# Kernel optimization log

Measured on AMD Instinct MI355X. Metric: run time of the kernel, lower is better.

## Reference

```python
import jax, jax.numpy as jnp
import numpy as np
from jax import lax

N = 51200            # total nodes
E = 409600           # edges
FEAT = 768           # BERT emb size
HID = 256            # GGNN out_channels
L = 6                # GGNN layers
NPG = 200            # nodes per graph (conv1d_1 in_channels)
C1_OUT, K1, P1 = 50, 3, 1
C2_OUT, K2 = 20, 1
MP1_K, MP1_S = 3, 2
MP2_K, MP2_S = 2, 2

def _pooled_len(n):
    n = (n - MP1_K) // MP1_S + 1
    n = (n - MP2_K) // MP2_S + 1
    return n

def setup_inputs():
    key = jax.random.key(0)
    ks = jax.random.split(key, 12)
    s = lambda i, shape: jax.random.normal(ks[i], shape, jnp.float32) * 0.02
    fc1_in = C2_OUT * _pooled_len(HID + FEAT)  # 20*255 = 5100
    fc2_in = C2_OUT * _pooled_len(HID)         # 20*63  = 1260
    return dict(
        x=jax.random.normal(ks[0], (N, FEAT), jnp.float32),
        edge_index=jax.random.randint(ks[1], (2, E), 0, N, dtype=jnp.int32),
        W_in=s(2, (HID, FEAT)), b_in=jnp.zeros((HID,), jnp.float32),
        W_ggnn=s(3, (L, HID, HID)),
        W_ih=s(4, (3 * HID, HID)), W_hh=s(5, (3 * HID, HID)),
        b_ih=jnp.zeros((3 * HID,), jnp.float32), b_hh=jnp.zeros((3 * HID,), jnp.float32),
        Wc1=s(6, (C1_OUT, NPG, K1)), bc1=jnp.zeros((C1_OUT,), jnp.float32),
        Wc2=s(7, (C2_OUT, C1_OUT, K2)), bc2=jnp.zeros((C2_OUT,), jnp.float32),
        Wf1=s(8, (1, fc1_in)), bf1=jnp.zeros((1,), jnp.float32),
        Wf2=s(9, (1, fc2_in)), bf2=jnp.zeros((1,), jnp.float32),
    )

def _conv1d(x, w, b, pad):
    y = lax.conv_general_dilated(x, w, (1,), [(pad, pad)], dimension_numbers=('NCH', 'OIH', 'NCH'))
    return y + b[None, :, None]

def _maxpool1d(x, k, s):
    return lax.reduce_window(x, -jnp.inf, lax.max, (1, 1, k), (1, 1, s), 'VALID')

def _ggnn(h0, src, dst, W_ggnn, W_ih, W_hh, b_ih, b_hh):
    h = h0
    for i in range(L):  # fixed small layer loop
        m = h @ W_ggnn[i]                                   # [N, HID]
        agg = jax.ops.segment_sum(m[src], dst, num_segments=N)  # scatter-add aggr
        gi = agg @ W_ih.T + b_ih                            # GRUCell input gates
        gh = h @ W_hh.T + b_hh                              # GRUCell hidden gates
        i_r, i_z, i_n = jnp.split(gi, 3, axis=1)
        h_r, h_z, h_n = jnp.split(gh, 3, axis=1)
        r = jax.nn.sigmoid(i_r + h_r)
        z = jax.nn.sigmoid(i_z + h_z)
        n = jnp.tanh(i_n + r * h_n)
        h = (1.0 - z) * n + z * h
    return h

def _conv_head(h, x, Wc1, bc1, Wc2, bc2, Wf1, bf1, Wf2, bf2):
    concat = jnp.concatenate([h, x], axis=1).reshape(-1, NPG, HID + FEAT)  # [G, NPG, 1024]
    Z = _maxpool1d(jax.nn.relu(_conv1d(concat, Wc1, bc1, P1)), MP1_K, MP1_S)
    Z = _maxpool1d(_conv1d(Z, Wc2, bc2, 0), MP2_K, MP2_S)
    Y = h.reshape(-1, NPG, HID)
    Y = _maxpool1d(jax.nn.relu(_conv1d(Y, Wc1, bc1, P1)), MP1_K, MP1_S)
    Y = _maxpool1d(_conv1d(Y, Wc2, bc2, 0), MP2_K, MP2_S)
    z = Z.reshape(Z.shape[0], -1) @ Wf1.T + bf1
    y = Y.reshape(Y.shape[0], -1) @ Wf2.T + bf2
    # dropout p=0.2 is identity in eval mode
    return jax.nn.sigmoid((z * y).ravel())  # [G]

def reference(x, edge_index, W_in, b_in, W_ggnn, W_ih, W_hh, b_ih, b_hh, Wc1, bc1, Wc2, bc2, Wf1, bf1, Wf2, bf2):
    h0 = x @ W_in.T + b_in
    h = _ggnn(h0, edge_index[0], edge_index[1], W_ggnn, W_ih, W_hh, b_ih, b_hh)
    p = _conv_head(h, x, Wc1, bc1, Wc2, bc2, Wf1, bf1, Wf2, bf2)
    eps = 1e-6
    p = jnp.clip(p, eps, 1.0 - eps)
    z1 = jnp.log(p / (1.0 - p))
    return jnp.stack([jnp.zeros_like(z1), z1], axis=1)  # [G, 2]
```

## Files before the change

kernel.cpp:

```cpp
#include <hip/hip_runtime.h>
#include <math.h>

#define N_NODES 51200
#define N_EDGES 409600
#define FEAT    768
#define HID     256
#define NPG     200
#define G_GRAPHS 256

typedef _Float16 f16x8 __attribute__((ext_vector_type(8)));
typedef _Float16 f16x4 __attribute__((ext_vector_type(4)));
typedef _Float16 f16x2 __attribute__((ext_vector_type(2)));
typedef float    f32x4 __attribute__((ext_vector_type(4)));

__global__ __launch_bounds__(256) void k_deg(const int* __restrict__ ei, int* __restrict__ deg) {
    int e = blockIdx.x * 256 + threadIdx.x;
    if (e < N_EDGES) atomicAdd(&deg[ei[N_EDGES + e]], 1);
}

__global__ __launch_bounds__(1024) void k_scan(const int* __restrict__ deg, int* __restrict__ rowp) {
    __shared__ int sums[1024];
    int tid = threadIdx.x;
    int base = tid * 50;
    int s = 0;
    for (int j = 0; j < 50; ++j) s += deg[base + j];
    sums[tid] = s;
    __syncthreads();
    for (int off = 1; off < 1024; off <<= 1) {
        int v = 0;
        if (tid >= off) v = sums[tid - off];
        __syncthreads();
        sums[tid] += v;
        __syncthreads();
    }
    int run = sums[tid] - s;
    for (int j = 0; j < 50; ++j) { rowp[base + j] = run; run += deg[base + j]; }
    if (tid == 1023) rowp[N_NODES] = run;
}

__global__ __launch_bounds__(256) void k_fill(const int* __restrict__ ei, const int* __restrict__ rowp,
                                              int* __restrict__ fill, int* __restrict__ col) {
    int e = blockIdx.x * 256 + threadIdx.x;
    if (e < N_EDGES) {
        int d = ei[N_EDGES + e];
        int pos = atomicAdd(&fill[d], 1);
        col[rowp[d] + pos] = ei[e];
    }
}

__global__ __launch_bounds__(256) void k_cvt(const float* __restrict__ in, _Float16* __restrict__ out, int n4) {
    int i = blockIdx.x * 256 + threadIdx.x;
    if (i < n4) {
        float4 v = *(const float4*)&in[i * 4];
        f16x4 h;
        h[0] = (_Float16)v.x; h[1] = (_Float16)v.y; h[2] = (_Float16)v.z; h[3] = (_Float16)v.w;
        *(f16x4*)&out[i * 4] = h;
    }
}

__global__ __launch_bounds__(256) void k_bias(const float* __restrict__ bih, const float* __restrict__ bhh,
                                              float* __restrict__ brz) {
    int i = blockIdx.x * 256 + threadIdx.x;
    if (i < 512) brz[i] = bih[i] + bhh[i];
}

__global__ __launch_bounds__(256) void k_bnn(const float* __restrict__ bih, const float* __restrict__ bhh,
                                             float* __restrict__ bnn) {
    int i = blockIdx.x * 256 + threadIdx.x;
    if (i < 512) bnn[i] = (i < 256) ? bih[512 + i] : bhh[512 + (i - 256)];
}

__global__ __launch_bounds__(256) void k_wpack(const float* __restrict__ Wc1, _Float16* __restrict__ Wp) {
    int id = blockIdx.x * 256 + threadIdx.x;
    int ch = id / 12288, r = id - ch * 12288;
    int o = r / 192, k = r - o * 192;
    int dk = k >> 6, cc = k & 63;
    int c = ch * 64 + cc;
    float v = 0.f;
    if (o < 50 && c < NPG) v = Wc1[(o * NPG + c) * 3 + dk];
    Wp[id] = (_Float16)v;
}

__global__ __launch_bounds__(256) void k_wcopyrz(const _Float16* __restrict__ Whh, _Float16* __restrict__ Wrz2) {
    int id = blockIdx.x * 256 + threadIdx.x;
    int l = id >> 17, r = id & 131071;
    int j = r >> 8, c = r & 255;
    Wrz2[(size_t)l * 262144 + j * 512 + 256 + c] = Whh[j * 256 + c];
}

__global__ __launch_bounds__(256) void k_wcopynn(const _Float16* __restrict__ Whh, _Float16* __restrict__ Wnn) {
    int id = blockIdx.x * 256 + threadIdx.x;
    int l = id >> 16, r = id & 65535;
    Wnn[(size_t)l * 131072 + 65536 + r] = Whh[512 * 256 + r];
}

template<int AF16, int OUT, int COLB, int SWZ>
__global__ __launch_bounds__(256) void k_gemm2(const void* __restrict__ Av, int lda,
                                               const _Float16* __restrict__ B,
                                               const float* __restrict__ bias,
                                               void* __restrict__ Cv, int ldc,
                                               _Float16* __restrict__ C2, int ldc2,
                                               int K, int wgPerL, int aLStride, int bLStride,
                                               int cLStride, int biasStride) {
    __shared__ _Float16 As[128 * 64];
    __shared__ _Float16 Bs[128 * 64];
    int wg = blockIdx.x;
    int l = wg / wgPerL; wg -= l * wgPerL;
    if (AF16) Av = (const void*)((const _Float16*)Av + (size_t)l * aLStride);
    else      Av = (const void*)((const float*)Av + (size_t)l * aLStride);
    B += (size_t)l * bLStride;
    if (bias) bias += (size_t)l * biasStride;
    if (OUT == 1) Cv = (void*)((_Float16*)Cv + (size_t)l * cLStride);
    else          Cv = (void*)((float*)Cv + (size_t)l * cLStride);
    int rowBase, colBase;
    if (SWZ) {
        int xcd = wg & 7, t = wg >> 3;
        int cb = t % COLB, gidx = t / COLB;
        rowBase = (gidx * 8 + xcd) * 128;
        colBase = cb * 128;
    } else {
        rowBase = (wg / COLB) * 128;
        colBase = (wg % COLB) * 128;
    }
    int tid = threadIdx.x;
    int lane = tid & 63;
    int wid = tid >> 6;
    int wr = wid >> 1, wc = wid & 1;
    f32x4 acc[4][4] = {};
    for (int k0 = 0; k0 < K; k0 += 64) {
        __syncthreads();
        #pragma unroll
        for (int p = 0; p < 4; ++p) {
            int c = p * 256 + tid;
            int row = c >> 3, slot = c & 7;
            int dst = row * 64 + ((slot ^ (row & 7)) * 8);
            if (AF16) {
                const _Float16* srcA = (const _Float16*)Av + (size_t)(rowBase + row) * lda + k0 + slot * 8;
                *(f16x8*)&As[dst] = *(const f16x8*)srcA;
            } else {
                const float* srcA = (const float*)Av + (size_t)(rowBase + row) * lda + k0 + slot * 8;
                float4 f0 = *(const float4*)srcA;
                float4 f1 = *(const float4*)(srcA + 4);
                f16x8 hv;
                hv[0] = (_Float16)f0.x; hv[1] = (_Float16)f0.y; hv[2] = (_Float16)f0.z; hv[3] = (_Float16)f0.w;
                hv[4] = (_Float16)f1.x; hv[5] = (_Float16)f1.y; hv[6] = (_Float16)f1.z; hv[7] = (_Float16)f1.w;
                *(f16x8*)&As[dst] = hv;
            }
            const _Float16* srcB = B + (size_t)(colBase + row) * K + k0 + slot * 8;
            *(f16x8*)&Bs[dst] = *(const f16x8*)srcB;
        }
        __syncthreads();
        #pragma unroll
        for (int ks = 0; ks < 2; ++ks) {
            f16x8 af[4], bf[4];
            #pragma unroll
            for (int mi = 0; mi < 4; ++mi) {
                int row = wr * 64 + mi * 16 + (lane & 15);
                int slot = (lane >> 4) + ks * 4;
                af[mi] = *(const f16x8*)&As[row * 64 + ((slot ^ (row & 7)) * 8)];
            }
            #pragma unroll
            for (int nj = 0; nj < 4; ++nj) {
                int row = wc * 64 + nj * 16 + (lane & 15);
                int slot = (lane >> 4) + ks * 4;
                bf[nj] = *(const f16x8*)&Bs[row * 64 + ((slot ^ (row & 7)) * 8)];
            }
            #pragma unroll
            for (int mi = 0; mi < 4; ++mi)
                #pragma unroll
                for (int nj = 0; nj < 4; ++nj)
                    acc[mi][nj] = __builtin_amdgcn_mfma_f32_16x16x32_f16(af[mi], bf[nj], acc[mi][nj], 0, 0, 0);
        }
    }
    #pragma unroll
    for (int mi = 0; mi < 4; ++mi) {
        #pragma unroll
        for (int nj = 0; nj < 4; ++nj) {
            int col = colBase + wc * 64 + nj * 16 + (lane & 15);
            float bv = bias ? bias[col] : 0.f;
            #pragma unroll
            for (int r = 0; r < 4; ++r) {
                int row = rowBase + wr * 64 + mi * 16 + (lane >> 4) * 4 + r;
                float val = acc[mi][nj][r] + bv;
                if (OUT == 0) {
                    ((float*)Cv)[(size_t)row * ldc + col] = val;
                } else if (OUT == 1) {
                    ((_Float16*)Cv)[(size_t)row * ldc + col] = (_Float16)val;
                } else {
                    ((float*)Cv)[(size_t)row * ldc + col] = val;
                    C2[(size_t)row * ldc2 + col] = (_Float16)val;
                }
            }
        }
    }
}

__global__ __launch_bounds__(256) void k_agg4(const int* __restrict__ rowp, const int* __restrict__ col,
                                              _Float16* __restrict__ AG) {
    int v = blockIdx.x * 4 + (threadIdx.x >> 6);
    int lane = threadIdx.x & 63;
    int beg = rowp[v], end = rowp[v + 1];
    const _Float16* hf = AG + 256 + lane * 4;
    float a0 = 0.f, a1 = 0.f, a2 = 0.f, a3 = 0.f;
    int i = beg;
    for (; i + 1 < end; i += 2) {
        f16x4 u = *(const f16x4*)&hf[(size_t)col[i] * 512];
        f16x4 w = *(const f16x4*)&hf[(size_t)col[i + 1] * 512];
        a0 += (float)u[0] + (float)w[0];
        a1 += (float)u[1] + (float)w[1];
        a2 += (float)u[2] + (float)w[2];
        a3 += (float)u[3] + (float)w[3];
    }
    if (i < end) {
        f16x4 u = *(const f16x4*)&hf[(size_t)col[i] * 512];
        a0 += (float)u[0]; a1 += (float)u[1]; a2 += (float)u[2]; a3 += (float)u[3];
    }
    f16x4 o;
    o[0] = (_Float16)a0; o[1] = (_Float16)a1; o[2] = (_Float16)a2; o[3] = (_Float16)a3;
    *(f16x4*)&AG[(size_t)v * 512 + lane * 4] = o;
}

__global__ __launch_bounds__(256) void k_gru4(const _Float16* __restrict__ gates, _Float16* __restrict__ AG) {
    int idx = blockIdx.x * 256 + threadIdx.x;
    int n = idx >> 5;
    int c8 = (idx & 31) << 3;
    size_t b = (size_t)n * 1024;
    f16x8 rp = *(const f16x8*)&gates[b + c8];
    f16x8 zp = *(const f16x8*)&gates[b + 256 + c8];
    f16x8 ip = *(const f16x8*)&gates[b + 512 + c8];
    f16x8 hp = *(const f16x8*)&gates[b + 768 + c8];
    f16x8 hv = *(const f16x8*)&AG[(size_t)n * 512 + 256 + c8];
    f16x8 ov;
    #pragma unroll
    for (int q = 0; q < 8; ++q) {
        float r = 1.f / (1.f + expf(-(float)rp[q]));
        float z = 1.f / (1.f + expf(-(float)zp[q]));
        float ng = tanhf((float)ip[q] + r * (float)hp[q]);
        float o = (1.f - z) * ng + z * (float)hv[q];
        ov[q] = (_Float16)o;
    }
    *(f16x8*)&AG[(size_t)n * 512 + 256 + c8] = ov;
}

__global__ __launch_bounds__(256, 2) void k_conv1m(const _Float16* __restrict__ hf, const _Float16* __restrict__ xf,
                                                   const _Float16* __restrict__ Wp, const float* __restrict__ bc1,
                                                   float* __restrict__ out, int H, int TBLK) {
    __shared__ _Float16 XT[272 * 64];
    __shared__ _Float16 WL[64 * 192];
    int g = blockIdx.x / TBLK;
    int tb = blockIdx.x - g * TBLK;
    int t0 = tb * 256;
    int tid = threadIdx.x;
    int lane = tid & 63;
    int wn = (tid >> 6) * 64;
    f32x4 acc[4][4] = {};
    for (int ch = 0; ch < 4; ++ch) {
        __syncthreads();
        #pragma unroll
        for (int i = 0; i < 6; ++i) {
            int q = i * 256 + tid;
            int o = q / 24, sk = q - o * 24;
            int skp = (sk & 0x18) | ((sk & 7) ^ (o & 7));
            *(f16x8*)&WL[o * 192 + skp * 8] = *(const f16x8*)&Wp[ch * 12288 + o * 192 + sk * 8];
        }
        for (int u = tid; u < 272; u += 256) {
            int r8 = u / 34, pc = u - r8 * 34;
            int gstart = t0 - 8 + pc * 8;
            int c0 = r8 * 8;
            f16x8 zv;
            #pragma unroll
            for (int q = 0; q < 8; ++q) zv[q] = (_Float16)0.f;
            f16x8 rows[8];
            if (gstart < 0 || gstart >= H) {
                #pragma unroll
                for (int j = 0; j < 8; ++j) rows[j] = zv;
            } else {
                const _Float16* base;
                int stride;
                if (gstart < HID) { base = hf + gstart; stride = 512; }
                else              { base = xf + (gstart - HID); stride = 768; }
                int node0 = g * NPG + ch * 64 + c0;
                #pragma unroll
                for (int j = 0; j < 8; ++j) {
                    int cg = ch * 64 + c0 + j;
                    rows[j] = (cg < NPG) ? *(const f16x8*)&base[(size_t)(node0 + j) * stride] : zv;
                }
            }
            #pragma unroll
            for (int jj = 0; jj < 8; ++jj) {
                f16x8 w;
                #pragma unroll
                for (int j = 0; j < 8; ++j) w[j] = rows[j][jj];
                int p = pc * 8 + jj;
                int slot = r8 ^ jj ^ (pc & 7);
                *(f16x8*)&XT[p * 64 + slot * 8] = w;
            }
        }
        __syncthreads();
        #pragma unroll
        for (int ks = 0; ks < 6; ++ks) {
            int dk = ks >> 1, cs0 = (ks & 1) << 2;
            f16x8 af[4], bf[4];
            #pragma unroll
            for (int mi = 0; mi < 4; ++mi) {
                int o = mi * 16 + (lane & 15);
                int sk = ks * 4 + (lane >> 4);
                int skp = (sk & 0x18) | ((sk & 7) ^ (o & 7));
                af[mi] = *(const f16x8*)&WL[o * 192 + skp * 8];
            }
            #pragma unroll
            for (int nj = 0; nj < 4; ++nj) {
                int tw = wn + nj * 16 + (lane & 15) + dk + 7;
                int sp = (cs0 + (lane >> 4)) ^ (tw & 7) ^ ((tw >> 3) & 7);
                bf[nj] = *(const f16x8*)&XT[tw * 64 + sp * 8];
            }
            #pragma unroll
            for (int mi = 0; mi < 4; ++mi)
                #pragma unroll
                for (int nj = 0; nj < 4; ++nj)
                    acc[mi][nj] = __builtin_amdgcn_mfma_f32_16x16x32_f16(af[mi], bf[nj], acc[mi][nj], 0, 0, 0);
        }
    }
    #pragma unroll
    for (int mi = 0; mi < 4; ++mi) {
        #pragma unroll
        for (int r = 0; r < 4; ++r) {
            int o = mi * 16 + (lane >> 4) * 4 + r;
            if (o < 50) {
                float b = bc1[o];
                #pragma unroll
                for (int nj = 0; nj < 4; ++nj) {
                    int t = t0 + wn + nj * 16 + (lane & 15);
                    float v = acc[mi][nj][r] + b;
                    out[(size_t)g * 50 * H + (size_t)o * H + t] = v > 0.f ? v : 0.f;
                }
            }
        }
    }
}

__global__ __launch_bounds__(256) void k_pool1(const float* __restrict__ in, float* __restrict__ out,
                                               int H, int U) {
    int g = blockIdx.x, o = blockIdx.y;
    const float* p = in + ((size_t)g * 50 + o) * H;
    float* q = out + ((size_t)g * 50 + o) * U;
    for (int u = threadIdx.x; u < U; u += 256) {
        float a = p[2 * u], b = p[2 * u + 1], c = p[2 * u + 2];
        float mm = a > b ? a : b;
        q[u] = mm > c ? mm : c;
    }
}

__global__ __launch_bounds__(256) void k_c2p2(const float* __restrict__ P1, const float* __restrict__ Wc2,
                                              const float* __restrict__ bc2, float* __restrict__ out,
                                              int U, int U2) {
    int g = blockIdx.x, o2 = blockIdx.y;
    float b = bc2[o2];
    for (int u2 = threadIdx.x; u2 < U2; u2 += 256) {
        float a0 = b, a1 = b;
        #pragma unroll 5
        for (int i = 0; i < 50; ++i) {
            float wv = Wc2[o2 * 50 + i];
            const float* p = P1 + ((size_t)g * 50 + i) * U + 2 * u2;
            a0 = fmaf(p[0], wv, a0);
            a1 = fmaf(p[1], wv, a1);
        }
        out[((size_t)g * 20 + o2) * U2 + u2] = a0 > a1 ? a0 : a1;
    }
}

__global__ __launch_bounds__(256) void k_fc(const float* __restrict__ P2, const float* __restrict__ Wf,
                                            const float* __restrict__ bf, float* __restrict__ out, int len) {
    __shared__ float red[256];
    int g = blockIdx.x, tid = threadIdx.x;
    const float* p = P2 + (size_t)g * len;
    float s = 0.f;
    for (int i = tid; i < len; i += 256) s = fmaf(p[i], Wf[i], s);
    red[tid] = s;
    __syncthreads();
    for (int off = 128; off > 0; off >>= 1) {
        if (tid < off) red[tid] += red[tid + off];
        __syncthreads();
    }
    if (tid == 0) out[g] = red[0] + bf[0];
}

__global__ __launch_bounds__(256) void k_final(const float* __restrict__ z, const float* __restrict__ y,
                                               float* __restrict__ out) {
    int g = threadIdx.x;
    float t = z[g] * y[g];
    float p = 1.f / (1.f + expf(-t));
    p = fminf(fmaxf(p, 1e-6f), 1.f - 1e-6f);
    float z1 = logf(p / (1.f - p));
    out[2 * g] = 0.f;
    out[2 * g + 1] = z1;
}

extern "C" void kernel_launch(void* const* d_in, const int* in_sizes, int n_in,
                              void* d_out, int out_size, void* d_ws, size_t ws_size,
                              hipStream_t stream) {
    const float* x     = (const float*)d_in[0];
    const int*   ei    = (const int*)d_in[1];
    const float* W_in  = (const float*)d_in[2];
    const float* b_in  = (const float*)d_in[3];
    const float* W_g   = (const float*)d_in[4];
    const float* W_ih  = (const float*)d_in[5];
    const float* W_hh  = (const float*)d_in[6];
    const float* b_ih  = (const float*)d_in[7];
    const float* b_hh  = (const float*)d_in[8];
    const float* Wc1   = (const float*)d_in[9];
    const float* bc1   = (const float*)d_in[10];
    const float* Wc2   = (const float*)d_in[11];
    const float* bc2   = (const float*)d_in[12];
    const float* Wf1   = (const float*)d_in[13];
    const float* bf1   = (const float*)d_in[14];
    const float* Wf2   = (const float*)d_in[15];
    const float* bf2   = (const float*)d_in[16];

    float* ws = (float*)d_ws;
    const size_t OFF_AG    = 0;
    const size_t OFF_GATES = 13107200;
    const size_t OFF_XF    = 39321600;
    const size_t OFF_WF    = 58982400;
    const size_t OFF_BRZ   = 60678144;
    const size_t OFF_BNN   = 60678656;
    const size_t OFF_INT   = 60679168;
    const size_t OFF_ZB    = 61242400;
    const size_t OFF_P2Z   = 61250000;
    const size_t OFF_P2Y   = 62600000;

    _Float16* AG      = (_Float16*)(ws + OFF_AG);
    _Float16* gates16 = (_Float16*)(ws + OFF_GATES);
    _Float16* XF      = (_Float16*)(ws + OFF_XF);

    _Float16* Win_h = (_Float16*)(ws + OFF_WF);
    _Float16* Wih_h = Win_h + 196608;
    _Float16* Whh_h = Wih_h + 196608;
    _Float16* Wg_h  = Whh_h + 196608;
    _Float16* Wrz2  = Wg_h  + 393216;
    _Float16* Wnn   = Wrz2  + 1572864;
    _Float16* Wp    = Wnn   + 786432;
    float* brz = ws + OFF_BRZ;
    float* bnn = ws + OFF_BNN;

    int* deg  = (int*)(ws + OFF_INT);
    int* fill = deg + N_NODES;
    int* rowp = fill + N_NODES;
    int* col  = rowp + (N_NODES + 1);
    float* zb = ws + OFF_ZB;
    float* yb = zb + 256;

    float* C1Z = ws + OFF_GATES;
    float* P1Z = ws + OFF_GATES + 13200000;
    float* C1Y = ws + OFF_GATES + 20000000;
    float* P1Y = ws + OFF_GATES + 23400000;
    float* P2Z = ws + OFF_P2Z;
    float* P2Y = ws + OFF_P2Y;

    k_cvt<<<192, 256, 0, stream>>>(W_in, Win_h, 49152);
    k_cvt<<<192, 256, 0, stream>>>(W_ih, Wih_h, 49152);
    k_cvt<<<192, 256, 0, stream>>>(W_hh, Whh_h, 49152);
    k_cvt<<<384, 256, 0, stream>>>(W_g, Wg_h, 98304);
    k_cvt<<<38400, 256, 0, stream>>>(x, XF, 9830400);
    k_bias<<<2, 256, 0, stream>>>(b_ih, b_hh, brz);
    k_bnn<<<2, 256, 0, stream>>>(b_ih, b_hh, bnn);
    k_wpack<<<192, 256, 0, stream>>>(Wc1, Wp);
    k_gemm2<1, 1, 2, 0><<<48, 256, 0, stream>>>(Wih_h, 256, Wg_h, nullptr,
                                                Wrz2, 512, nullptr, 0, 256, 8, 0, 65536, 262144, 0);
    k_gemm2<1, 1, 2, 0><<<24, 256, 0, stream>>>(Wih_h + 512 * 256, 256, Wg_h, nullptr,
                                                Wnn, 256, nullptr, 0, 256, 4, 0, 65536, 131072, 0);
    k_wcopyrz<<<3072, 256, 0, stream>>>(Whh_h, Wrz2);
    k_wcopynn<<<1536, 256, 0, stream>>>(Whh_h, Wnn);

    hipMemsetAsync(deg, 0, N_NODES * sizeof(int), stream);
    hipMemsetAsync(fill, 0, N_NODES * sizeof(int), stream);
    k_deg<<<N_EDGES / 256, 256, 0, stream>>>(ei, deg);
    k_scan<<<1, 1024, 0, stream>>>(deg, rowp);
    k_fill<<<N_EDGES / 256, 256, 0, stream>>>(ei, rowp, fill, col);

    k_gemm2<0, 1, 2, 1><<<800, 256, 0, stream>>>(x, FEAT, Win_h, b_in, AG + 256, 512,
                                                 nullptr, 0, FEAT, 800, 0, 0, 0, 0);

    for (int l = 0; l < 6; ++l) {
        k_agg4<<<12800, 256, 0, stream>>>(rowp, col, AG);
        k_gemm2<1, 1, 4, 1><<<1600, 256, 0, stream>>>(AG, 512, Wrz2 + (size_t)l * 262144, brz,
                                                      gates16, 1024, nullptr, 0, 512, 1600, 0, 0, 0, 0);
        k_gemm2<1, 1, 2, 1><<<1600, 256, 0, stream>>>(AG, 512, Wnn + (size_t)l * 131072, bnn,
                                                      gates16 + 512, 1024, nullptr, 0, 256,
                                                      800, 256, 65536, 256, 256);
        k_gru4<<<6400, 256, 0, stream>>>(gates16, AG);
    }

    k_conv1m<<<1024, 256, 0, stream>>>(AG + 256, XF, Wp, bc1, C1Z, 1024, 4);
    k_pool1<<<dim3(G_GRAPHS, 50), 256, 0, stream>>>(C1Z, P1Z, 1024, 511);
    k_c2p2<<<dim3(G_GRAPHS, 20), 256, 0, stream>>>(P1Z, Wc2, bc2, P2Z, 511, 255);
    k_fc<<<G_GRAPHS, 256, 0, stream>>>(P2Z, Wf1, bf1, zb, 20 * 255);

    k_conv1m<<<256, 256, 0, stream>>>(AG + 256, XF, Wp, bc1, C1Y, 256, 1);
    k_pool1<<<dim3(G_GRAPHS, 50), 256, 0, stream>>>(C1Y, P1Y, 256, 127);
    k_c2p2<<<dim3(G_GRAPHS, 20), 256, 0, stream>>>(P1Y, Wc2, bc2, P2Y, 127, 63);
    k_fc<<<G_GRAPHS, 256, 0, stream>>>(P2Y, Wf2, bf2, yb, 20 * 63);

    k_final<<<1, 256, 0, stream>>>(zb, yb, (float*)d_out);
}
```

Measured before the change: 1.223 ms.

## Fuse GRU n-gate GEMMs with elementwise update and ping-pong hidden buffers

Replaces the interleaved AG buffer with separate aggregate and hidden-state buffers, ping-ponging the hidden state across layers. The n-gate input and hidden GEMMs run as two accumulators in a single 512-thread kernel whose epilogue applies the full GRU update, removing the separate gate-write and k_gru4 pass. The rz GEMM now reads its A operand from two separate buffers, and the first projection uses the pre-converted fp16 x. This cuts gate-buffer traffic and launches, at the cost of larger shared memory and more registers in the fused kernel.

```diff
diff --git a/kernel.cpp b/kernel.cpp
--- a/kernel.cpp
+++ b/kernel.cpp
@@ -10,7 +10,6 @@
 
 typedef _Float16 f16x8 __attribute__((ext_vector_type(8)));
 typedef _Float16 f16x4 __attribute__((ext_vector_type(4)));
-typedef _Float16 f16x2 __attribute__((ext_vector_type(2)));
 typedef float    f32x4 __attribute__((ext_vector_type(4)));
 
 __global__ __launch_bounds__(256) void k_deg(const int* __restrict__ ei, int* __restrict__ deg) {
@@ -88,18 +87,11 @@
     Wrz2[(size_t)l * 262144 + j * 512 + 256 + c] = Whh[j * 256 + c];
 }
 
-__global__ __launch_bounds__(256) void k_wcopynn(const _Float16* __restrict__ Whh, _Float16* __restrict__ Wnn) {
-    int id = blockIdx.x * 256 + threadIdx.x;
-    int l = id >> 16, r = id & 65535;
-    Wnn[(size_t)l * 131072 + 65536 + r] = Whh[512 * 256 + r];
-}
-
 template<int AF16, int OUT, int COLB, int SWZ>
 __global__ __launch_bounds__(256) void k_gemm2(const void* __restrict__ Av, int lda,
                                                const _Float16* __restrict__ B,
                                                const float* __restrict__ bias,
                                                void* __restrict__ Cv, int ldc,
-                                               _Float16* __restrict__ C2, int ldc2,
                                                int K, int wgPerL, int aLStride, int bLStride,
                                                int cLStride, int biasStride) {
     __shared__ _Float16 As[128 * 64];
@@ -182,64 +174,183 @@
             for (int r = 0; r < 4; ++r) {
                 int row = rowBase + wr * 64 + mi * 16 + (lane >> 4) * 4 + r;
                 float val = acc[mi][nj][r] + bv;
-                if (OUT == 0) {
-                    ((float*)Cv)[(size_t)row * ldc + col] = val;
-                } else if (OUT == 1) {
-                    ((_Float16*)Cv)[(size_t)row * ldc + col] = (_Float16)val;
-                } else {
-                    ((float*)Cv)[(size_t)row * ldc + col] = val;
-                    C2[(size_t)row * ldc2 + col] = (_Float16)val;
+                if (OUT == 0) ((float*)Cv)[(size_t)row * ldc + col] = val;
+                else          ((_Float16*)Cv)[(size_t)row * ldc + col] = (_Float16)val;
+            }
+        }
+    }
+}
+
+__global__ __launch_bounds__(256) void k_gemmrz(const _Float16* __restrict__ S, const _Float16* __restrict__ hc,
+                                                const _Float16* __restrict__ B, const float* __restrict__ bias,
+                                                _Float16* __restrict__ C) {
+    __shared__ _Float16 As[128 * 64];
+    __shared__ _Float16 Bs[128 * 64];
+    int wg = blockIdx.x;
+    int xcd = wg & 7, t = wg >> 3;
+    int cb = t % 4, gidx = t / 4;
+    int rowBase = (gidx * 8 + xcd) * 128;
+    int colBase = cb * 128;
+    int tid = threadIdx.x;
+    int lane = tid & 63;
+    int wid = tid >> 6;
+    int wr = wid >> 1, wc = wid & 1;
+    f32x4 acc[4][4] = {};
+    for (int k0 = 0; k0 < 512; k0 += 64) {
+        const _Float16* Abase = (k0 < 256) ? S : hc;
+        int kk = k0 & 255;
+        __syncthreads();
+        #pragma unroll
+        for (int p = 0; p < 4; ++p) {
+            int c = p * 256 + tid;
+            int row = c >> 3, slot = c & 7;
+            int dst = row * 64 + ((slot ^ (row & 7)) * 8);
+            *(f16x8*)&As[dst] = *(const f16x8*)&Abase[(size_t)(rowBase + row) * 256 + kk + slot * 8];
+            *(f16x8*)&Bs[dst] = *(const f16x8*)&B[(size_t)(colBase + row) * 512 + k0 + slot * 8];
+        }
+        __syncthreads();
+        #pragma unroll
+        for (int ks = 0; ks < 2; ++ks) {
+            f16x8 af[4], bf[4];
+            #pragma unroll
+            for (int mi = 0; mi < 4; ++mi) {
+                int row = wr * 64 + mi * 16 + (lane & 15);
+                int slot = (lane >> 4) + ks * 4;
+                af[mi] = *(const f16x8*)&As[row * 64 + ((slot ^ (row & 7)) * 8)];
+            }
+            #pragma unroll
+            for (int nj = 0; nj < 4; ++nj) {
+                int row = wc * 64 + nj * 16 + (lane & 15);
+                int slot = (lane >> 4) + ks * 4;
+                bf[nj] = *(const f16x8*)&Bs[row * 64 + ((slot ^ (row & 7)) * 8)];
+            }
+            #pragma unroll
+            for (int mi = 0; mi < 4; ++mi)
+                #pragma unroll
+                for (int nj = 0; nj < 4; ++nj)
+                    acc[mi][nj] = __builtin_amdgcn_mfma_f32_16x16x32_f16(af[mi], bf[nj], acc[mi][nj], 0, 0, 0);
+        }
+    }
+    #pragma unroll
+    for (int mi = 0; mi < 4; ++mi) {
+        #pragma unroll
+        for (int nj = 0; nj < 4; ++nj) {
+            int col = colBase + wc * 64 + nj * 16 + (lane & 15);
+            float bv = bias[col];
+            #pragma unroll
+            for (int r = 0; r < 4; ++r) {
+                int row = rowBase + wr * 64 + mi * 16 + (lane >> 4) * 4 + r;
+                C[(size_t)row * 512 + col] = (_Float16)(acc[mi][nj][r] + bv);
+            }
+        }
+    }
+}
+
+__global__ __launch_bounds__(512) void k_nngru(const _Float16* __restrict__ S, const _Float16* __restrict__ hc,
+                                               const _Float16* __restrict__ B0, const _Float16* __restrict__ B1,
+                                               const float* __restrict__ bnn, const _Float16* __restrict__ rz,
+                                               _Float16* __restrict__ hn) {
+    __shared__ _Float16 As0[128 * 64], As1[128 * 64], Bs0[128 * 64], Bs1[128 * 64];
+    int wg = blockIdx.x;
+    int xcd = wg & 7, t = wg >> 3;
+    int cb = t % 2, gidx = t / 2;
+    int rowBase = (gidx * 8 + xcd) * 128;
+    int colBase = cb * 128;
+    int tid = threadIdx.x;
+    int lane = tid & 63;
+    int wid = tid >> 6;
+    int wr = wid >> 2, wc = wid & 3;
+    f32x4 acc0[4][2] = {}, acc1[4][2] = {};
+    for (int k0 = 0; k0 < 256; k0 += 64) {
+        __syncthreads();
+        #pragma unroll
+        for (int p = 0; p < 8; ++p) {
+            int q = p * 512 + tid;
+            int tile = q >> 10;
+            int c = q & 1023;
+            int row = c >> 3, slot = c & 7;
+            int dst = row * 64 + ((slot ^ (row & 7)) * 8);
+            const _Float16* src;
+            _Float16* d;
+            if (tile == 0)      { src = S  + (size_t)(rowBase + row) * 256 + k0 + slot * 8; d = As0; }
+            else if (tile == 1) { src = hc + (size_t)(rowBase + row) * 256 + k0 + slot * 8; d = As1; }
+            else if (tile == 2) { src = B0 + (size_t)(colBase + row) * 256 + k0 + slot * 8; d = Bs0; }
+            else                { src = B1 + (size_t)(colBase + row) * 256 + k0 + slot * 8; d = Bs1; }
+            *(f16x8*)&d[dst] = *(const f16x8*)src;
+        }
+        __syncthreads();
+        #pragma unroll
+        for (int ks = 0; ks < 2; ++ks) {
+            f16x8 a0[4], a1[4], b0[2], b1[2];
+            #pragma unroll
+            for (int mi = 0; mi < 4; ++mi) {
+                int row = wr * 64 + mi * 16 + (lane & 15);
+                int slot = (lane >> 4) + ks * 4;
+                int off = row * 64 + ((slot ^ (row & 7)) * 8);
+                a0[mi] = *(const f16x8*)&As0[off];
+                a1[mi] = *(const f16x8*)&As1[off];
+            }
+            #pragma unroll
+            for (int nj = 0; nj < 2; ++nj) {
+                int row = wc * 32 + nj * 16 + (lane & 15);
+                int slot = (lane >> 4) + ks * 4;
+                int off = row * 64 + ((slot ^ (row & 7)) * 8);
+                b0[nj] = *(const f16x8*)&Bs0[off];
+                b1[nj] = *(const f16x8*)&Bs1[off];
+            }
+            #pragma unroll
+            for (int mi = 0; mi < 4; ++mi)
+                #pragma unroll
+                for (int nj = 0; nj < 2; ++nj) {
+                    acc0[mi][nj] = __builtin_amdgcn_mfma_f32_16x16x32_f16(a0[mi], b0[nj], acc0[mi][nj], 0, 0, 0);
+                    acc1[mi][nj] = __builtin_amdgcn_mfma_f32_16x16x32_f16(a1[mi], b1[nj], acc1[mi][nj], 0, 0, 0);
                 }
+        }
+    }
+    #pragma unroll
+    for (int mi = 0; mi < 4; ++mi) {
+        #pragma unroll
+        for (int nj = 0; nj < 2; ++nj) {
+            int col = colBase + wc * 32 + nj * 16 + (lane & 15);
+            float bi = bnn[col], bh = bnn[256 + col];
+            #pragma unroll
+            for (int r = 0; r < 4; ++r) {
+                int row = rowBase + wr * 64 + mi * 16 + (lane >> 4) * 4 + r;
+                float rv = (float)rz[(size_t)row * 512 + col];
+                float zv = (float)rz[(size_t)row * 512 + 256 + col];
+                float rg = 1.f / (1.f + expf(-rv));
+                float zg = 1.f / (1.f + expf(-zv));
+                float ng = tanhf((acc0[mi][nj][r] + bi) + rg * (acc1[mi][nj][r] + bh));
+                float ho = (float)hc[(size_t)row * 256 + col];
+                hn[(size_t)row * 256 + col] = (_Float16)((1.f - zg) * ng + zg * ho);
             }
         }
     }
 }
 
 __global__ __launch_bounds__(256) void k_agg4(const int* __restrict__ rowp, const int* __restrict__ col,
-                                              _Float16* __restrict__ AG) {
+                                              const _Float16* __restrict__ hc, _Float16* __restrict__ S) {
     int v = blockIdx.x * 4 + (threadIdx.x >> 6);
     int lane = threadIdx.x & 63;
     int beg = rowp[v], end = rowp[v + 1];
-    const _Float16* hf = AG + 256 + lane * 4;
+    const _Float16* hf = hc + lane * 4;
     float a0 = 0.f, a1 = 0.f, a2 = 0.f, a3 = 0.f;
     int i = beg;
     for (; i + 1 < end; i += 2) {
-        f16x4 u = *(const f16x4*)&hf[(size_t)col[i] * 512];
-        f16x4 w = *(const f16x4*)&hf[(size_t)col[i + 1] * 512];
+        f16x4 u = *(const f16x4*)&hf[(size_t)col[i] * 256];
+        f16x4 w = *(const f16x4*)&hf[(size_t)col[i + 1] * 256];
         a0 += (float)u[0] + (float)w[0];
         a1 += (float)u[1] + (float)w[1];
         a2 += (float)u[2] + (float)w[2];
         a3 += (float)u[3] + (float)w[3];
     }
     if (i < end) {
-        f16x4 u = *(const f16x4*)&hf[(size_t)col[i] * 512];
+        f16x4 u = *(const f16x4*)&hf[(size_t)col[i] * 256];
         a0 += (float)u[0]; a1 += (float)u[1]; a2 += (float)u[2]; a3 += (float)u[3];
     }
     f16x4 o;
     o[0] = (_Float16)a0; o[1] = (_Float16)a1; o[2] = (_Float16)a2; o[3] = (_Float16)a3;
-    *(f16x4*)&AG[(size_t)v * 512 + lane * 4] = o;
-}
-
-__global__ __launch_bounds__(256) void k_gru4(const _Float16* __restrict__ gates, _Float16* __restrict__ AG) {
-    int idx = blockIdx.x * 256 + threadIdx.x;
-    int n = idx >> 5;
-    int c8 = (idx & 31) << 3;
-    size_t b = (size_t)n * 1024;
-    f16x8 rp = *(const f16x8*)&gates[b + c8];
-    f16x8 zp = *(const f16x8*)&gates[b + 256 + c8];
-    f16x8 ip = *(const f16x8*)&gates[b + 512 + c8];
-    f16x8 hp = *(const f16x8*)&gates[b + 768 + c8];
-    f16x8 hv = *(const f16x8*)&AG[(size_t)n * 512 + 256 + c8];
-    f16x8 ov;
-    #pragma unroll
-    for (int q = 0; q < 8; ++q) {
-        float r = 1.f / (1.f + expf(-(float)rp[q]));
-        float z = 1.f / (1.f + expf(-(float)zp[q]));
-        float ng = tanhf((float)ip[q] + r * (float)hp[q]);
-        float o = (1.f - z) * ng + z * (float)hv[q];
-        ov[q] = (_Float16)o;
-    }
-    *(f16x8*)&AG[(size_t)n * 512 + 256 + c8] = ov;
+    *(f16x4*)&S[(size_t)v * 256 + lane * 4] = o;
 }
 
 __global__ __launch_bounds__(256, 2) void k_conv1m(const _Float16* __restrict__ hf, const _Float16* __restrict__ xf,
@@ -277,7 +388,7 @@
             } else {
                 const _Float16* base;
                 int stride;
-                if (gstart < HID) { base = hf + gstart; stride = 512; }
+                if (gstart < HID) { base = hf + gstart; stride = 256; }
                 else              { base = xf + (gstart - HID); stride = 768; }
                 int node0 = g * NPG + ch * 64 + c0;
                 #pragma unroll
@@ -418,28 +529,33 @@
     const float* bf2   = (const float*)d_in[16];
 
     float* ws = (float*)d_ws;
-    const size_t OFF_AG    = 0;
-    const size_t OFF_GATES = 13107200;
-    const size_t OFF_XF    = 39321600;
-    const size_t OFF_WF    = 58982400;
-    const size_t OFF_BRZ   = 60678144;
-    const size_t OFF_BNN   = 60678656;
-    const size_t OFF_INT   = 60679168;
-    const size_t OFF_ZB    = 61242400;
-    const size_t OFF_P2Z   = 61250000;
-    const size_t OFF_P2Y   = 62600000;
-
-    _Float16* AG      = (_Float16*)(ws + OFF_AG);
-    _Float16* gates16 = (_Float16*)(ws + OFF_GATES);
-    _Float16* XF      = (_Float16*)(ws + OFF_XF);
+    const size_t OFF_S   = 0;
+    const size_t OFF_HA  = 6553600;
+    const size_t OFF_HB  = 13107200;
+    const size_t OFF_RZ  = 19660800;
+    const size_t OFF_XF  = 32768000;
+    const size_t OFF_WF  = 52428800;
+    const size_t OFF_BRZ = 53927936;
+    const size_t OFF_BNN = 53928448;
+    const size_t OFF_INT = 53928960;
+    const size_t OFF_ZB  = 54492200;
+    const size_t OFF_P2Z = 54500000;
+    const size_t OFF_P2Y = 55900000;
+
+    _Float16* S  = (_Float16*)(ws + OFF_S);
+    _Float16* HA = (_Float16*)(ws + OFF_HA);
+    _Float16* HB = (_Float16*)(ws + OFF_HB);
+    _Float16* RZ = (_Float16*)(ws + OFF_RZ);
+    _Float16* XF = (_Float16*)(ws + OFF_XF);
 
     _Float16* Win_h = (_Float16*)(ws + OFF_WF);
     _Float16* Wih_h = Win_h + 196608;
     _Float16* Whh_h = Wih_h + 196608;
     _Float16* Wg_h  = Whh_h + 196608;
     _Float16* Wrz2  = Wg_h  + 393216;
-    _Float16* Wnn   = Wrz2  + 1572864;
-    _Float16* Wp    = Wnn   + 786432;
+    _Float16* Wni2  = Wrz2  + 1572864;
+    _Float16* Wp    = Wni2  + 393216;
+    _Float16* Whhn  = Whh_h + 512 * 256;
     float* brz = ws + OFF_BRZ;
     float* bnn = ws + OFF_BNN;
 
@@ -450,10 +566,10 @@
     float* zb = ws + OFF_ZB;
     float* yb = zb + 256;
 
-    float* C1Z = ws + OFF_GATES;
-    float* P1Z = ws + OFF_GATES + 13200000;
-    float* C1Y = ws + OFF_GATES + 20000000;
-    float* P1Y = ws + OFF_GATES + 23400000;
+    float* C1Z = ws + OFF_RZ;
+    float* P1Z = ws + OFF_HB;
+    float* C1Y = ws + OFF_S;
+    float* P1Y = ws + 3300000;
     float* P2Z = ws + OFF_P2Z;
     float* P2Y = ws + OFF_P2Y;
 
@@ -466,11 +582,10 @@
     k_bnn<<<2, 256, 0, stream>>>(b_ih, b_hh, bnn);
     k_wpack<<<192, 256, 0, stream>>>(Wc1, Wp);
     k_gemm2<1, 1, 2, 0><<<48, 256, 0, stream>>>(Wih_h, 256, Wg_h, nullptr,
-                                                Wrz2, 512, nullptr, 0, 256, 8, 0, 65536, 262144, 0);
+                                                Wrz2, 512, 256, 8, 0, 65536, 262144, 0);
     k_gemm2<1, 1, 2, 0><<<24, 256, 0, stream>>>(Wih_h + 512 * 256, 256, Wg_h, nullptr,
-                                                Wnn, 256, nullptr, 0, 256, 4, 0, 65536, 131072, 0);
+                                                Wni2, 256, 256, 4, 0, 65536, 65536, 0);
     k_wcopyrz<<<3072, 256, 0, stream>>>(Whh_h, Wrz2);
-    k_wcopynn<<<1536, 256, 0, stream>>>(Whh_h, Wnn);
 
     hipMemsetAsync(deg, 0, N_NODES * sizeof(int), stream);
     hipMemsetAsync(fill, 0, N_NODES * sizeof(int), stream);
@@ -478,25 +593,23 @@
     k_scan<<<1, 1024, 0, stream>>>(deg, rowp);
     k_fill<<<N_EDGES / 256, 256, 0, stream>>>(ei, rowp, fill, col);
 
-    k_gemm2<0, 1, 2, 1><<<800, 256, 0, stream>>>(x, FEAT, Win_h, b_in, AG + 256, 512,
-                                                 nullptr, 0, FEAT, 800, 0, 0, 0, 0);
+    k_gemm2<1, 1, 2, 1><<<800, 256, 0, stream>>>(XF, FEAT, Win_h, b_in, HA, HID,
+                                                 FEAT, 800, 0, 0, 0, 0);
 
     for (int l = 0; l < 6; ++l) {
-        k_agg4<<<12800, 256, 0, stream>>>(rowp, col, AG);
-        k_gemm2<1, 1, 4, 1><<<1600, 256, 0, stream>>>(AG, 512, Wrz2 + (size_t)l * 262144, brz,
-                                                      gates16, 1024, nullptr, 0, 512, 1600, 0, 0, 0, 0);
-        k_gemm2<1, 1, 2, 1><<<1600, 256, 0, stream>>>(AG, 512, Wnn + (size_t)l * 131072, bnn,
-                                                      gates16 + 512, 1024, nullptr, 0, 256,
-                                                      800, 256, 65536, 256, 256);
-        k_gru4<<<6400, 256, 0, stream>>>(gates16, AG);
-    }
-
-    k_conv1m<<<1024, 256, 0, stream>>>(AG + 256, XF, Wp, bc1, C1Z, 1024, 4);
+        _Float16* hc = (l & 1) ? HB : HA;
+        _Float16* hn = (l & 1) ? HA : HB;
+        k_agg4<<<12800, 256, 0, stream>>>(rowp, col, hc, S);
+        k_gemmrz<<<1600, 256, 0, stream>>>(S, hc, Wrz2 + (size_t)l * 262144, brz, RZ);
+        k_nngru<<<800, 512, 0, stream>>>(S, hc, Wni2 + (size_t)l * 65536, Whhn, bnn, RZ, hn);
+    }
+
+    k_conv1m<<<1024, 256, 0, stream>>>(HA, XF, Wp, bc1, C1Z, 1024, 4);
     k_pool1<<<dim3(G_GRAPHS, 50), 256, 0, stream>>>(C1Z, P1Z, 1024, 511);
     k_c2p2<<<dim3(G_GRAPHS, 20), 256, 0, stream>>>(P1Z, Wc2, bc2, P2Z, 511, 255);
     k_fc<<<G_GRAPHS, 256, 0, stream>>>(P2Z, Wf1, bf1, zb, 20 * 255);
 
-    k_conv1m<<<256, 256, 0, stream>>>(AG + 256, XF, Wp, bc1, C1Y, 256, 1);
+    k_conv1m<<<256, 256, 0, stream>>>(HA, XF, Wp, bc1, C1Y, 256, 1);
     k_pool1<<<dim3(G_GRAPHS, 50), 256, 0, stream>>>(C1Y, P1Y, 256, 127);
     k_c2p2<<<dim3(G_GRAPHS, 20), 256, 0, stream>>>(P1Y, Wc2, bc2, P2Y, 127, 63);
     k_fc<<<G_GRAPHS, 256, 0, stream>>>(P2Y, Wf2, bf2, yb, 20 * 63);
```

New measurement: 1.213 ms. Within noise of the previous version (-0.9%).
